# Performance work log

Measured on AMD Instinct MI355X. Metric: run time of the kernel, lower is better.

## Reference

```python
import jax, jax.numpy as jnp
import numpy as np

BN_EPS = 1e-5


def _conv(x, w, stride, pad):
    return jax.lax.conv_general_dilated(
        x, w, (stride, stride), [(pad, pad), (pad, pad)],
        dimension_numbers=('NCHW', 'OIHW', 'NCHW'))


def setup_inputs() -> dict:
    key = jax.random.key(0)
    ks = jax.random.split(key, 6)
    b, c, h, w = 8, 32, 80, 160
    guidance = jax.random.normal(ks[0], (b, c, 2 * h, 2 * w), dtype=jnp.float32)
    # positive disparities, realistic magnitude
    disp = jax.random.uniform(ks[1], (b, 1, h, w), dtype=jnp.float32) * 24.0
    conv1_w = jax.random.normal(ks[2], (2 * c, c, 3, 3), dtype=jnp.float32) * 0.05
    bn_gamma = jnp.ones((2 * c,), dtype=jnp.float32)
    bn_beta = jnp.zeros((2 * c,), dtype=jnp.float32)
    bn_mean = jax.random.normal(ks[3], (2 * c,), dtype=jnp.float32) * 0.1
    bn_var = jax.random.uniform(ks[4], (2 * c,), dtype=jnp.float32, minval=0.5, maxval=1.5)
    conv2_w = jax.random.normal(ks[5], (9 * 64, 2 * c, 3, 3), dtype=jnp.float32) * 0.05
    return {'guidance': guidance, 'disp': disp, 'conv1_w': conv1_w,
            'bn_gamma': bn_gamma, 'bn_beta': bn_beta, 'bn_mean': bn_mean,
            'bn_var': bn_var, 'conv2_w': conv2_w}


def reference(guidance, disp, conv1_w, bn_gamma, bn_beta, bn_mean, bn_var, conv2_w):
    b, _, h, w = disp.shape
    # mask branch: convbn(stride 2) + ReLU + conv -> 9*64 channels at (h, w)
    x = _conv(guidance, conv1_w, 2, 1)
    inv = jax.lax.rsqrt(bn_var + BN_EPS)
    x = (x - bn_mean[None, :, None, None]) * (inv * bn_gamma)[None, :, None, None] + bn_beta[None, :, None, None]
    x = jax.nn.relu(x)
    mask = _conv(x, conv2_w, 1, 1).reshape(b, 1, 9, 8, 8, h, w)
    mask = jax.nn.softmax(mask, axis=2)
    # unfold(8*disp, 3x3, pad=1) -> (b, 1, 9, h, w), row-major kernel order
    d8 = jnp.pad(8.0 * disp, ((0, 0), (0, 0), (1, 1), (1, 1)))
    patches = jnp.stack([d8[:, :, i:i + h, j:j + w]
                         for i in range(3) for j in range(3)], axis=2)
    # convex combination over the 9 neighbors
    up = jnp.sum(mask * patches[:, :, :, None, None], axis=2)  # (b,1,8,8,h,w)
    up = up.transpose(0, 1, 4, 2, 5, 3)  # (b,1,h,8,w,8)
    return up.reshape(b, 1, 8 * h, 8 * w)
```

## Files before the change

### kernel.cpp

```cpp
#include <hip/hip_runtime.h>
#include <math.h>

typedef _Float16 half8 __attribute__((ext_vector_type(8)));
typedef float f32x4 __attribute__((ext_vector_type(4)));

constexpr int B_ = 8;
constexpr int HG = 160, WG = 320;
constexpr int H = 80, W = 160;
constexpr size_t CWS_OFF  = 0;
constexpr size_t W1WS_OFF = 663552;
constexpr size_t XG_OFF   = 700416;
constexpr size_t CNT_OFF  = 13807616;

__global__ __launch_bounds__(256) void prep(const float* __restrict__ w1,
                                            const float* __restrict__ w2,
                                            char* __restrict__ ws)
{
    int e = blockIdx.x * 256 + threadIdx.x;
    if (e < 576 * 64) {
        int n = e >> 6, cin = e & 63;
        int k = n >> 6, ng = (n >> 4) & 3, nl = n & 15;
        int kl = cin & 31, c5 = cin >> 5;
        const float* src = w2 + ((size_t)(n * 64 + cin)) * 9;
        int fragoff = ((kl >> 3) * 16 + nl) * 16 + (kl & 7) * 2;
#pragma unroll
        for (int t = 0; t < 9; ++t) {
            int s = t * 2 + c5;
            *(_Float16*)(ws + CWS_OFF + (size_t)ng * 165888
                         + (size_t)(s * 9 + k) * 1024 + fragoff) = (_Float16)src[t];
        }
    } else if (e < 576 * 64 + 64 * 32) {
        int e2 = e - 576 * 64;
        int ch = e2 >> 5, cin = e2 & 31;
        const float* src = w1 + ((size_t)(ch * 32 + cin)) * 9;
        int fragoff = (ch >> 4) * 1024 + ((cin >> 3) * 16 + (ch & 15)) * 16 + (cin & 7) * 2;
#pragma unroll
        for (int t = 0; t < 9; ++t)
            *(_Float16*)(ws + W1WS_OFF + (size_t)t * 4096 + fragoff) = (_Float16)src[t];
    }
}

__global__ __launch_bounds__(256, 4) void conv1_mfma(
    const float* __restrict__ g, const char* __restrict__ ws_w1,
    const float* __restrict__ gamma, const float* __restrict__ beta,
    const float* __restrict__ mean, const float* __restrict__ var,
    _Float16* __restrict__ xg)
{
    const int tx0 = blockIdx.x * 16, ty0 = blockIdx.y * 8, b = blockIdx.z;
    __shared__ __align__(16) _Float16 gl[2][17][18][32];
    const int tid = threadIdx.x;

    const int gy0 = 2 * ty0 - 1;
    const int gxa0 = 2 * tx0 - 2;
    for (int i = tid; i < 17 * 32 * 17; i += 256) {
        int wr = i / 544; int rem = i - wr * 544;
        int cin = rem / 17; int c2 = rem - cin * 17;
        int gy = gy0 + wr;
        int gxa = gxa0 + 2 * c2;
        float2 v = make_float2(0.f, 0.f);
        if (gy >= 0 && gy < HG && gxa >= 0)
            v = *(const float2*)(g + ((size_t)(b * 32 + cin) * HG + gy) * WG + gxa);
        int slot = cin >> 3, elem = cin & 7;
        if (c2 > 0) {
            int wch = c2 - 1;
            gl[1][wr][wch][((slot ^ ((wch >> 1) & 3)) << 3) + elem] = (_Float16)v.x;
        }
        {
            int wch = c2;
            gl[0][wr][wch][((slot ^ ((wch >> 1) & 3)) << 3) + elem] = (_Float16)v.y;
        }
    }

    const int lane = tid & 63, w = tid >> 6;
    const int c = lane & 15, grp = lane >> 4;

    const _Float16* w1p = (const _Float16*)ws_w1 + lane * 8;
    half8 bf[4];
#pragma unroll
    for (int nt = 0; nt < 4; ++nt) bf[nt] = *(const half8*)(w1p + nt * 512);

    f32x4 zf = {0.f, 0.f, 0.f, 0.f};
    f32x4 acc[2][4];
#pragma unroll
    for (int mt = 0; mt < 2; ++mt)
#pragma unroll
        for (int nt = 0; nt < 4; ++nt) acc[mt][nt] = zf;

    __syncthreads();

#pragma unroll
    for (int s = 0; s < 9; ++s) {
        const int dy = s / 3, dx = s - dy * 3;
        const int par = dx & 1, dxh = dx >> 1;
        half8 af[2];
#pragma unroll
        for (int mt = 0; mt < 2; ++mt) {
            int wr = 2 * (2 * w + mt) + dy;
            int wch = c + dxh;
            af[mt] = *(const half8*)&gl[par][wr][wch][(grp ^ ((wch >> 1) & 3)) << 3];
        }
        const _Float16* wnext = w1p + (size_t)(s + 1) * 2048;
#pragma unroll
        for (int nt = 0; nt < 4; ++nt) {
            half8 cur = bf[nt];
            bf[nt] = *(const half8*)(wnext + nt * 512);
            acc[0][nt] = __builtin_amdgcn_mfma_f32_16x16x32_f16(af[0], cur, acc[0][nt], 0, 0, 0);
            acc[1][nt] = __builtin_amdgcn_mfma_f32_16x16x32_f16(af[1], cur, acc[1][nt], 0, 0, 0);
        }
    }

#pragma unroll
    for (int nt = 0; nt < 4; ++nt) {
        int ch = nt * 16 + c;
        float mu = mean[ch], scv = rsqrtf(var[ch] + 1e-5f) * gamma[ch], bt = beta[ch];
#pragma unroll
        for (int mt = 0; mt < 2; ++mt) {
            int y = ty0 + 2 * w + mt;
#pragma unroll
            for (int r = 0; r < 4; ++r) {
                int x = tx0 + grp * 4 + r;
                float v = fmaxf((acc[mt][nt][r] - mu) * scv + bt, 0.f);
                xg[(((size_t)(b * H + y) * W + x) << 6) + ch] = (_Float16)v;
            }
        }
    }
}

__global__ __launch_bounds__(256, 2) void conv2_mfma(
    const _Float16* __restrict__ xg, const char* __restrict__ ws_c,
    const float* __restrict__ disp, float* __restrict__ out,
    int* __restrict__ cnt)
{
    __shared__ __align__(16) _Float16 xs[108 * 64];
    __shared__ float d8s[108];
    __shared__ int s_tile;
    const int tid = threadIdx.x;
    const int lane = tid & 63, wid = tid >> 6;
    const int c = lane & 15, grp = lane >> 4;

    const _Float16* wp = (const _Float16*)ws_c + (size_t)wid * 82944 + lane * 8;

    half8 zero8;
#pragma unroll
    for (int j = 0; j < 8; ++j) zero8[j] = (_Float16)0.f;

    for (;;) {
        if (tid == 0) s_tile = atomicAdd(cnt, 1);
        __syncthreads();
        const int tile = __builtin_amdgcn_readfirstlane(s_tile);
        if (tile >= 1600) break;
        const int b   = tile / 200;
        const int rem = tile - b * 200;
        const int tyi = rem / 10;
        const int tx0 = (rem - tyi * 10) * 16, ty0 = tyi * 4;

        for (int cidx = tid; cidx < 864; cidx += 256) {
            int wpx = cidx >> 3, slot = cidx & 7;
            int rr = wpx / 18, cc = wpx - rr * 18;
            int y = ty0 - 1 + rr, xc = tx0 - 1 + cc;
            half8 v = zero8;
            if (y >= 0 && y < H && xc >= 0 && xc < W)
                v = *(const half8*)(xg + (((size_t)(b * H + y) * W + xc) << 6) + slot * 8);
            *(half8*)&xs[wpx * 64 + (slot ^ (wpx & 7)) * 8] = v;
        }
        if (tid < 108) {
            int rr = tid / 18, cc = tid - rr * 18;
            int y = ty0 - 1 + rr, xc = tx0 - 1 + cc;
            float v = 0.f;
            if (y >= 0 && y < H && xc >= 0 && xc < W) v = 8.f * disp[(b * H + y) * W + xc];
            d8s[tid] = v;
        }

        f32x4 zf = {0.f, 0.f, 0.f, 0.f};
        f32x4 acc[4][9];
#pragma unroll
        for (int m = 0; m < 4; ++m)
#pragma unroll
            for (int k = 0; k < 9; ++k) acc[m][k] = zf;

        half8 bf[9];
#pragma unroll
        for (int k = 0; k < 9; ++k) bf[k] = *(const half8*)(wp + k * 512);

        __syncthreads();

#pragma unroll 2
        for (int s = 0; s < 18; ++s) {
            const int t = s >> 1;
            const int dy = t / 3, dx = t - dy * 3;
            const int aslot = (s & 1) * 4 + grp;
            half8 af[4];
#pragma unroll
            for (int mt = 0; mt < 4; ++mt) {
                int wrow = (mt + dy) * 18 + c + dx;
                af[mt] = *(const half8*)&xs[wrow * 64 + (aslot ^ (wrow & 7)) * 8];
            }
            const _Float16* wnext = wp + (size_t)(s + 1) * 4608;
#pragma unroll
            for (int k = 0; k < 9; ++k) {
                half8 cur = bf[k];
                bf[k] = *(const half8*)(wnext + k * 512);
#pragma unroll
                for (int mt = 0; mt < 4; ++mt)
                    acc[mt][k] = __builtin_amdgcn_mfma_f32_16x16x32_f16(
                        af[mt], cur, acc[mt][k], 0, 0, 0);
            }
        }

        const int ij = wid * 16 + c;
        const int oi = ij >> 3, oj = ij & 7;
#pragma unroll
        for (int mt = 0; mt < 4; ++mt) {
#pragma unroll
            for (int r = 0; r < 4; ++r) {
                int pr = mt, pc = grp * 4 + r;
                float pat[9];
#pragma unroll
                for (int k9 = 0; k9 < 9; ++k9) pat[k9] = d8s[(pr + k9 / 3) * 18 + pc + k9 % 3];
                float mx = acc[mt][0][r];
#pragma unroll
                for (int k9 = 1; k9 < 9; ++k9) mx = fmaxf(mx, acc[mt][k9][r]);
                float sum = 0.f, up = 0.f;
#pragma unroll
                for (int k9 = 0; k9 < 9; ++k9) {
                    float e = __expf(acc[mt][k9][r] - mx);
                    sum += e; up += e * pat[k9];
                }
                int y = ty0 + pr, xc = tx0 + pc;
                out[((size_t)(b * (8 * H) + y * 8 + oi)) * (size_t)(8 * W) + xc * 8 + oj] = up / sum;
            }
        }
    }
}

extern "C" void kernel_launch(void* const* d_in, const int* in_sizes, int n_in,
                              void* d_out, int out_size, void* d_ws, size_t ws_size,
                              hipStream_t stream)
{
    const float* guidance = (const float*)d_in[0];
    const float* disp     = (const float*)d_in[1];
    const float* conv1_w  = (const float*)d_in[2];
    const float* bn_gamma = (const float*)d_in[3];
    const float* bn_beta  = (const float*)d_in[4];
    const float* bn_mean  = (const float*)d_in[5];
    const float* bn_var   = (const float*)d_in[6];
    const float* conv2_w  = (const float*)d_in[7];
    float* out = (float*)d_out;
    char* ws = (char*)d_ws;
    _Float16* xg = (_Float16*)(ws + XG_OFF);
    int* cnt = (int*)(ws + CNT_OFF);

    hipMemsetAsync(cnt, 0, sizeof(int), stream);
    prep<<<dim3((576 * 64 + 64 * 32 + 255) / 256), dim3(256), 0, stream>>>(
        conv1_w, conv2_w, ws);
    dim3 grid1(W / 16, H / 8, B_);
    conv1_mfma<<<grid1, dim3(256), 0, stream>>>(
        guidance, ws + W1WS_OFF, bn_gamma, bn_beta, bn_mean, bn_var, xg);
    conv2_mfma<<<dim3(1024), dim3(256), 0, stream>>>(
        xg, ws + CWS_OFF, disp, out, cnt);
}
```

Baseline: 124.2 us.

## Pack softmax taps into MFMA N dimension and split tiles for higher occupancy

```diff
diff --git a/kernel.cpp b/kernel.cpp
--- a/kernel.cpp
+++ b/kernel.cpp
@@ -8,9 +8,9 @@
 constexpr int HG = 160, WG = 320;
 constexpr int H = 80, W = 160;
 constexpr size_t CWS_OFF  = 0;
-constexpr size_t W1WS_OFF = 663552;
-constexpr size_t XG_OFF   = 700416;
-constexpr size_t CNT_OFF  = 13807616;
+constexpr size_t W1WS_OFF = 737280;
+constexpr size_t XG_OFF   = 774144;
+constexpr size_t CNT_OFF  = 13881344;
 
 __global__ __launch_bounds__(256) void prep(const float* __restrict__ w1,
                                             const float* __restrict__ w2,
@@ -19,15 +19,20 @@
     int e = blockIdx.x * 256 + threadIdx.x;
     if (e < 576 * 64) {
         int n = e >> 6, cin = e & 63;
-        int k = n >> 6, ng = (n >> 4) & 3, nl = n & 15;
-        int kl = cin & 31, c5 = cin >> 5;
+        int k = n >> 6;
+        int ij = n & 63;
+        int ng = ij >> 3, ijl = ij & 7;
+        int f = k >> 1, kp = k & 1;
+        int cc = ijl * 2 + kp;
+        int grp = (cin & 31) >> 3, j = cin & 7;
+        int c5 = cin >> 5;
         const float* src = w2 + ((size_t)(n * 64 + cin)) * 9;
-        int fragoff = ((kl >> 3) * 16 + nl) * 16 + (kl & 7) * 2;
+        size_t base = CWS_OFF + (size_t)ng * 92160 + (size_t)f * 1024
+                    + (grp * 16 + cc) * 16 + j * 2;
 #pragma unroll
         for (int t = 0; t < 9; ++t) {
             int s = t * 2 + c5;
-            *(_Float16*)(ws + CWS_OFF + (size_t)ng * 165888
-                         + (size_t)(s * 9 + k) * 1024 + fragoff) = (_Float16)src[t];
+            *(_Float16*)(ws + base + (size_t)s * 5120) = (_Float16)src[t];
         }
     } else if (e < 576 * 64 + 64 * 32) {
         int e2 = e - 576 * 64;
@@ -37,6 +42,16 @@
 #pragma unroll
         for (int t = 0; t < 9; ++t)
             *(_Float16*)(ws + W1WS_OFF + (size_t)t * 4096 + fragoff) = (_Float16)src[t];
+    } else if (e < 576 * 64 + 64 * 32 + 4608) {
+        int e3 = e - (576 * 64 + 64 * 32);
+        int ng = e3 / 576, rem = e3 - ng * 576;
+        int s = rem >> 5, idx = rem & 31;
+        int grp = idx >> 3, codd = ((idx & 7) << 1) | 1;
+        half8 z;
+#pragma unroll
+        for (int q = 0; q < 8; ++q) z[q] = (_Float16)0.f;
+        *(half8*)(ws + CWS_OFF + (size_t)ng * 92160 + (size_t)s * 5120
+                  + 4 * 1024 + (grp * 16 + codd) * 16) = z;
     }
 }
 
@@ -126,7 +141,7 @@
     }
 }
 
-__global__ __launch_bounds__(256, 2) void conv2_mfma(
+__global__ __launch_bounds__(256, 3) void conv2_mfma(
     const _Float16* __restrict__ xg, const char* __restrict__ ws_c,
     const float* __restrict__ disp, float* __restrict__ out,
     int* __restrict__ cnt)
@@ -137,8 +152,7 @@
     const int tid = threadIdx.x;
     const int lane = tid & 63, wid = tid >> 6;
     const int c = lane & 15, grp = lane >> 4;
-
-    const _Float16* wp = (const _Float16*)ws_c + (size_t)wid * 82944 + lane * 8;
+    const int kp = c & 1, ijl = c >> 1;
 
     half8 zero8;
 #pragma unroll
@@ -148,39 +162,43 @@
         if (tid == 0) s_tile = atomicAdd(cnt, 1);
         __syncthreads();
         const int tile = __builtin_amdgcn_readfirstlane(s_tile);
-        if (tile >= 1600) break;
-        const int b   = tile / 200;
-        const int rem = tile - b * 200;
+        if (tile >= 3200) break;
+        const int pxt = tile >> 1, h = tile & 1;
+        const int b   = pxt / 200;
+        const int rem = pxt - b * 200;
         const int tyi = rem / 10;
         const int tx0 = (rem - tyi * 10) * 16, ty0 = tyi * 4;
+        const int ng  = h * 4 + wid;
 
         for (int cidx = tid; cidx < 864; cidx += 256) {
             int wpx = cidx >> 3, slot = cidx & 7;
-            int rr = wpx / 18, cc = wpx - rr * 18;
-            int y = ty0 - 1 + rr, xc = tx0 - 1 + cc;
+            int rr = wpx / 18, cc2 = wpx - rr * 18;
+            int y = ty0 - 1 + rr, xc = tx0 - 1 + cc2;
             half8 v = zero8;
             if (y >= 0 && y < H && xc >= 0 && xc < W)
                 v = *(const half8*)(xg + (((size_t)(b * H + y) * W + xc) << 6) + slot * 8);
             *(half8*)&xs[wpx * 64 + (slot ^ (wpx & 7)) * 8] = v;
         }
         if (tid < 108) {
-            int rr = tid / 18, cc = tid - rr * 18;
-            int y = ty0 - 1 + rr, xc = tx0 - 1 + cc;
+            int rr = tid / 18, cc2 = tid - rr * 18;
+            int y = ty0 - 1 + rr, xc = tx0 - 1 + cc2;
             float v = 0.f;
             if (y >= 0 && y < H && xc >= 0 && xc < W) v = 8.f * disp[(b * H + y) * W + xc];
             d8s[tid] = v;
         }
 
         f32x4 zf = {0.f, 0.f, 0.f, 0.f};
-        f32x4 acc[4][9];
+        f32x4 acc[4][5];
 #pragma unroll
         for (int m = 0; m < 4; ++m)
 #pragma unroll
-            for (int k = 0; k < 9; ++k) acc[m][k] = zf;
-
-        half8 bf[9];
-#pragma unroll
-        for (int k = 0; k < 9; ++k) bf[k] = *(const half8*)(wp + k * 512);
+            for (int f = 0; f < 5; ++f) acc[m][f] = zf;
+
+        const _Float16* wp = (const _Float16*)ws_c + (size_t)ng * 46080 + lane * 8;
+
+        half8 bf[5];
+#pragma unroll
+        for (int f = 0; f < 5; ++f) bf[f] = *(const half8*)(wp + f * 512);
 
         __syncthreads();
 
@@ -195,39 +213,51 @@
                 int wrow = (mt + dy) * 18 + c + dx;
                 af[mt] = *(const half8*)&xs[wrow * 64 + (aslot ^ (wrow & 7)) * 8];
             }
-            const _Float16* wnext = wp + (size_t)(s + 1) * 4608;
-#pragma unroll
-            for (int k = 0; k < 9; ++k) {
-                half8 cur = bf[k];
-                bf[k] = *(const half8*)(wnext + k * 512);
+            const _Float16* wnext = wp + (size_t)(s + 1) * 2560;
+#pragma unroll
+            for (int f = 0; f < 5; ++f) {
+                half8 cur = bf[f];
+                bf[f] = *(const half8*)(wnext + f * 512);
 #pragma unroll
                 for (int mt = 0; mt < 4; ++mt)
-                    acc[mt][k] = __builtin_amdgcn_mfma_f32_16x16x32_f16(
-                        af[mt], cur, acc[mt][k], 0, 0, 0);
-            }
-        }
-
-        const int ij = wid * 16 + c;
-        const int oi = ij >> 3, oj = ij & 7;
+                    acc[mt][f] = __builtin_amdgcn_mfma_f32_16x16x32_f16(
+                        af[mt], cur, acc[mt][f], 0, 0, 0);
+            }
+        }
+
+        const int oi = ng;
+        const int oj = ijl;
+        const bool v4 = (kp == 0);
 #pragma unroll
         for (int mt = 0; mt < 4; ++mt) {
 #pragma unroll
             for (int r = 0; r < 4; ++r) {
-                int pr = mt, pc = grp * 4 + r;
-                float pat[9];
-#pragma unroll
-                for (int k9 = 0; k9 < 9; ++k9) pat[k9] = d8s[(pr + k9 / 3) * 18 + pc + k9 % 3];
-                float mx = acc[mt][0][r];
-#pragma unroll
-                for (int k9 = 1; k9 < 9; ++k9) mx = fmaxf(mx, acc[mt][k9][r]);
-                float sum = 0.f, up = 0.f;
-#pragma unroll
-                for (int k9 = 0; k9 < 9; ++k9) {
-                    float e = __expf(acc[mt][k9][r] - mx);
-                    sum += e; up += e * pat[k9];
+                const int pc = grp * 4 + r;
+                float a4 = v4 ? acc[mt][4][r] : -3.0e38f;
+                float mxo = fmaxf(fmaxf(fmaxf(acc[mt][0][r], acc[mt][1][r]),
+                                        fmaxf(acc[mt][2][r], acc[mt][3][r])), a4);
+                float oth = __int_as_float(__builtin_amdgcn_ds_swizzle(
+                    __float_as_int(mxo), 0x041F));
+                float mx = fmaxf(mxo, oth);
+                float so = 0.f, uo = 0.f;
+#pragma unroll
+                for (int f = 0; f < 5; ++f) {
+                    int k = 2 * f + kp;
+                    int kk = (k < 9) ? k : 8;
+                    float e = __expf(acc[mt][f][r] - mx);
+                    if (f == 4) e = v4 ? e : 0.f;
+                    float pkf = d8s[(mt + kk / 3) * 18 + pc + kk % 3];
+                    so += e; uo += e * pkf;
                 }
-                int y = ty0 + pr, xc = tx0 + pc;
-                out[((size_t)(b * (8 * H) + y * 8 + oi)) * (size_t)(8 * W) + xc * 8 + oj] = up / sum;
+                float sum = so + __int_as_float(__builtin_amdgcn_ds_swizzle(
+                    __float_as_int(so), 0x041F));
+                float up  = uo + __int_as_float(__builtin_amdgcn_ds_swizzle(
+                    __float_as_int(uo), 0x041F));
+                if (kp == 0) {
+                    int y = ty0 + mt, xc = tx0 + pc;
+                    out[((size_t)(b * (8 * H) + y * 8 + oi)) * (size_t)(8 * W)
+                        + xc * 8 + oj] = up / sum;
+                }
             }
         }
     }
@@ -251,11 +281,11 @@
     int* cnt = (int*)(ws + CNT_OFF);
 
     hipMemsetAsync(cnt, 0, sizeof(int), stream);
-    prep<<<dim3((576 * 64 + 64 * 32 + 255) / 256), dim3(256), 0, stream>>>(
+    prep<<<dim3((576 * 64 + 64 * 32 + 4608 + 255) / 256), dim3(256), 0, stream>>>(
         conv1_w, conv2_w, ws);
     dim3 grid1(W / 16, H / 8, B_);
     conv1_mfma<<<grid1, dim3(256), 0, stream>>>(
         guidance, ws + W1WS_OFF, bn_gamma, bn_beta, bn_mean, bn_var, xg);
-    conv2_mfma<<<dim3(1024), dim3(256), 0, stream>>>(
+    conv2_mfma<<<dim3(1536), dim3(256), 0, stream>>>(
         xg, ws + CWS_OFF, disp, out, cnt);
 }
```

New measurement: 147.2 us. +18.5%, slower.

## Replace atomic tile scheduler with static grid and staggered weight-phase start

Applied to the files above, without the earlier changes.

```diff
diff --git a/kernel.cpp b/kernel.cpp
--- a/kernel.cpp
+++ b/kernel.cpp
@@ -10,7 +10,6 @@
 constexpr size_t CWS_OFF  = 0;
 constexpr size_t W1WS_OFF = 663552;
 constexpr size_t XG_OFF   = 700416;
-constexpr size_t CNT_OFF  = 13807616;
 
 __global__ __launch_bounds__(256) void prep(const float* __restrict__ w1,
                                             const float* __restrict__ w2,
@@ -128,107 +127,100 @@
 
 __global__ __launch_bounds__(256, 2) void conv2_mfma(
     const _Float16* __restrict__ xg, const char* __restrict__ ws_c,
-    const float* __restrict__ disp, float* __restrict__ out,
-    int* __restrict__ cnt)
-{
+    const float* __restrict__ disp, float* __restrict__ out)
+{
+    const int tx0 = blockIdx.x * 16, ty0 = blockIdx.y * 4, b = blockIdx.z;
     __shared__ __align__(16) _Float16 xs[108 * 64];
     __shared__ float d8s[108];
-    __shared__ int s_tile;
     const int tid = threadIdx.x;
     const int lane = tid & 63, wid = tid >> 6;
     const int c = lane & 15, grp = lane >> 4;
 
+    half8 zero8;
+#pragma unroll
+    for (int j = 0; j < 8; ++j) zero8[j] = (_Float16)0.f;
+    for (int cidx = tid; cidx < 864; cidx += 256) {
+        int wpx = cidx >> 3, slot = cidx & 7;
+        int rr = wpx / 18, cc = wpx - rr * 18;
+        int y = ty0 - 1 + rr, xc = tx0 - 1 + cc;
+        half8 v = zero8;
+        if (y >= 0 && y < H && xc >= 0 && xc < W)
+            v = *(const half8*)(xg + (((size_t)(b * H + y) * W + xc) << 6) + slot * 8);
+        *(half8*)&xs[wpx * 64 + (slot ^ (wpx & 7)) * 8] = v;
+    }
+    if (tid < 108) {
+        int rr = tid / 18, cc = tid - rr * 18;
+        int y = ty0 - 1 + rr, xc = tx0 - 1 + cc;
+        float v = 0.f;
+        if (y >= 0 && y < H && xc >= 0 && xc < W) v = 8.f * disp[(b * H + y) * W + xc];
+        d8s[tid] = v;
+    }
+
+    f32x4 zf = {0.f, 0.f, 0.f, 0.f};
+    f32x4 acc[4][9];
+#pragma unroll
+    for (int m = 0; m < 4; ++m)
+#pragma unroll
+        for (int k = 0; k < 9; ++k) acc[m][k] = zf;
+
     const _Float16* wp = (const _Float16*)ws_c + (size_t)wid * 82944 + lane * 8;
 
-    half8 zero8;
-#pragma unroll
-    for (int j = 0; j < 8; ++j) zero8[j] = (_Float16)0.f;
-
-    for (;;) {
-        if (tid == 0) s_tile = atomicAdd(cnt, 1);
-        __syncthreads();
-        const int tile = __builtin_amdgcn_readfirstlane(s_tile);
-        if (tile >= 1600) break;
-        const int b   = tile / 200;
-        const int rem = tile - b * 200;
-        const int tyi = rem / 10;
-        const int tx0 = (rem - tyi * 10) * 16, ty0 = tyi * 4;
-
-        for (int cidx = tid; cidx < 864; cidx += 256) {
-            int wpx = cidx >> 3, slot = cidx & 7;
-            int rr = wpx / 18, cc = wpx - rr * 18;
-            int y = ty0 - 1 + rr, xc = tx0 - 1 + cc;
-            half8 v = zero8;
-            if (y >= 0 && y < H && xc >= 0 && xc < W)
-                v = *(const half8*)(xg + (((size_t)(b * H + y) * W + xc) << 6) + slot * 8);
-            *(half8*)&xs[wpx * 64 + (slot ^ (wpx & 7)) * 8] = v;
-        }
-        if (tid < 108) {
-            int rr = tid / 18, cc = tid - rr * 18;
-            int y = ty0 - 1 + rr, xc = tx0 - 1 + cc;
-            float v = 0.f;
-            if (y >= 0 && y < H && xc >= 0 && xc < W) v = 8.f * disp[(b * H + y) * W + xc];
-            d8s[tid] = v;
-        }
-
-        f32x4 zf = {0.f, 0.f, 0.f, 0.f};
-        f32x4 acc[4][9];
-#pragma unroll
-        for (int m = 0; m < 4; ++m)
-#pragma unroll
-            for (int k = 0; k < 9; ++k) acc[m][k] = zf;
-
-        half8 bf[9];
-#pragma unroll
-        for (int k = 0; k < 9; ++k) bf[k] = *(const half8*)(wp + k * 512);
-
-        __syncthreads();
-
+    const int lb = (blockIdx.z * 20 + blockIdx.y) * 10 + blockIdx.x;
+    const int s0 = (lb * 7) % 18;
+
+    half8 bf[9];
+#pragma unroll
+    for (int k = 0; k < 9; ++k) bf[k] = *(const half8*)(wp + (size_t)s0 * 4608 + k * 512);
+
+    __syncthreads();
+
+    int s = s0;
 #pragma unroll 2
-        for (int s = 0; s < 18; ++s) {
-            const int t = s >> 1;
-            const int dy = t / 3, dx = t - dy * 3;
-            const int aslot = (s & 1) * 4 + grp;
-            half8 af[4];
-#pragma unroll
-            for (int mt = 0; mt < 4; ++mt) {
-                int wrow = (mt + dy) * 18 + c + dx;
-                af[mt] = *(const half8*)&xs[wrow * 64 + (aslot ^ (wrow & 7)) * 8];
+    for (int i = 0; i < 18; ++i) {
+        int sn = s + 1; if (sn == 18) sn = 0;
+        const int t = s >> 1;
+        const int dy = t / 3, dx = t - dy * 3;
+        const int aslot = (s & 1) * 4 + grp;
+        half8 af[4];
+#pragma unroll
+        for (int mt = 0; mt < 4; ++mt) {
+            int wrow = (mt + dy) * 18 + c + dx;
+            af[mt] = *(const half8*)&xs[wrow * 64 + (aslot ^ (wrow & 7)) * 8];
+        }
+        const _Float16* wnext = wp + (size_t)sn * 4608;
+#pragma unroll
+        for (int k = 0; k < 9; ++k) {
+            half8 cur = bf[k];
+            bf[k] = *(const half8*)(wnext + k * 512);
+#pragma unroll
+            for (int mt = 0; mt < 4; ++mt)
+                acc[mt][k] = __builtin_amdgcn_mfma_f32_16x16x32_f16(
+                    af[mt], cur, acc[mt][k], 0, 0, 0);
+        }
+        s = sn;
+    }
+
+    const int ij = wid * 16 + c;
+    const int oi = ij >> 3, oj = ij & 7;
+#pragma unroll
+    for (int mt = 0; mt < 4; ++mt) {
+#pragma unroll
+        for (int r = 0; r < 4; ++r) {
+            int pr = mt, pc = grp * 4 + r;
+            float pat[9];
+#pragma unroll
+            for (int k9 = 0; k9 < 9; ++k9) pat[k9] = d8s[(pr + k9 / 3) * 18 + pc + k9 % 3];
+            float mx = acc[mt][0][r];
+#pragma unroll
+            for (int k9 = 1; k9 < 9; ++k9) mx = fmaxf(mx, acc[mt][k9][r]);
+            float sum = 0.f, up = 0.f;
+#pragma unroll
+            for (int k9 = 0; k9 < 9; ++k9) {
+                float e = __expf(acc[mt][k9][r] - mx);
+                sum += e; up += e * pat[k9];
             }
-            const _Float16* wnext = wp + (size_t)(s + 1) * 4608;
-#pragma unroll
-            for (int k = 0; k < 9; ++k) {
-                half8 cur = bf[k];
-                bf[k] = *(const half8*)(wnext + k * 512);
-#pragma unroll
-                for (int mt = 0; mt < 4; ++mt)
-                    acc[mt][k] = __builtin_amdgcn_mfma_f32_16x16x32_f16(
-                        af[mt], cur, acc[mt][k], 0, 0, 0);
-            }
-        }
-
-        const int ij = wid * 16 + c;
-        const int oi = ij >> 3, oj = ij & 7;
-#pragma unroll
-        for (int mt = 0; mt < 4; ++mt) {
-#pragma unroll
-            for (int r = 0; r < 4; ++r) {
-                int pr = mt, pc = grp * 4 + r;
-                float pat[9];
-#pragma unroll
-                for (int k9 = 0; k9 < 9; ++k9) pat[k9] = d8s[(pr + k9 / 3) * 18 + pc + k9 % 3];
-                float mx = acc[mt][0][r];
-#pragma unroll
-                for (int k9 = 1; k9 < 9; ++k9) mx = fmaxf(mx, acc[mt][k9][r]);
-                float sum = 0.f, up = 0.f;
-#pragma unroll
-                for (int k9 = 0; k9 < 9; ++k9) {
-                    float e = __expf(acc[mt][k9][r] - mx);
-                    sum += e; up += e * pat[k9];
-                }
-                int y = ty0 + pr, xc = tx0 + pc;
-                out[((size_t)(b * (8 * H) + y * 8 + oi)) * (size_t)(8 * W) + xc * 8 + oj] = up / sum;
-            }
+            int y = ty0 + pr, xc = tx0 + pc;
+            out[((size_t)(b * (8 * H) + y * 8 + oi)) * (size_t)(8 * W) + xc * 8 + oj] = up / sum;
         }
     }
 }
@@ -248,14 +240,13 @@
     float* out = (float*)d_out;
     char* ws = (char*)d_ws;
     _Float16* xg = (_Float16*)(ws + XG_OFF);
-    int* cnt = (int*)(ws + CNT_OFF);
-
-    hipMemsetAsync(cnt, 0, sizeof(int), stream);
+
     prep<<<dim3((576 * 64 + 64 * 32 + 255) / 256), dim3(256), 0, stream>>>(
         conv1_w, conv2_w, ws);
     dim3 grid1(W / 16, H / 8, B_);
     conv1_mfma<<<grid1, dim3(256), 0, stream>>>(
         guidance, ws + W1WS_OFF, bn_gamma, bn_beta, bn_mean, bn_var, xg);
-    conv2_mfma<<<dim3(1024), dim3(256), 0, stream>>>(
-        xg, ws + CWS_OFF, disp, out, cnt);
-}
+    dim3 grid2(W / 16, H / 4, B_);
+    conv2_mfma<<<grid2, dim3(256), 0, stream>>>(
+        xg, ws + CWS_OFF, disp, out);
+}
```

Measured after the change: 110.8 us. -10.8%, faster.
